# Kernel optimization log

Hardware: AMD Instinct MI355X
Metric: run time of the kernel (lower is better)

## Reference

```python
import jax, jax.numpy as jnp
import numpy as np

N, C, D = 8192, 16, 5

def setup_inputs() -> dict:
    key = jax.random.key(0)
    k1, k2 = jax.random.split(key)
    U = jax.random.normal(k1, (N, C), dtype=jnp.float32)
    ref = jax.random.normal(k2, (N, D), dtype=jnp.float32)
    return {"U": U, "ref": ref}

def reference(U, ref):
    # Exact Gaussian bilateral filter that the permutohedral lattice approximates:
    # out_i = sum_j exp(-0.5 * ||ref_i - ref_j||^2) * U_j  -  U_i
    sq = jnp.sum(ref * ref, axis=-1)                      # [N]
    # squared pairwise distances via gram trick: ||ri||^2 + ||rj||^2 - 2 ri.rj
    d2 = sq[:, None] + sq[None, :] - 2.0 * (ref @ ref.T)  # [N, N]
    W = jnp.exp(-0.5 * jnp.maximum(d2, 0.0))              # [N, N] Gaussian kernel
    return W @ U - U                                      # [N, C]
```

## Files before the change

kernel.cpp:

```cpp
#include <hip/hip_runtime.h>


#define N_ROWS 8192
#define C_CH   16
#define D_DIM  5
#define TPB    256
#define MI     4
#define IPB    (TPB * MI)
#define NIB    (N_ROWS / IPB)
#define NSEG   64
#define JPB    (N_ROWS / NSEG)

#if __has_builtin(__builtin_amdgcn_exp2f)
#define EXP2(x) __builtin_amdgcn_exp2f(x)
#else
#define EXP2(x) exp2f(x)
#endif

#define LOG2E 1.4426950408889634f

__global__ __launch_bounds__(TPB) void lg_main(const float* __restrict__ U,
                                               const float* __restrict__ ref,
                                               float* __restrict__ part) {
    __shared__ float sj[JPB][8];
    __shared__ float su[JPB][16];

    const int bid = blockIdx.x;
    const int ib  = bid % NIB;
    const int seg = bid / NIB;
    const int tid = threadIdx.x;
    const int j0  = seg * JPB;

    const int ibase = ib * IPB + tid;
    float r[MI][D_DIM];
#pragma unroll
    for (int q = 0; q < MI; ++q) {
        const int i = ibase + q * TPB;
#pragma unroll
        for (int d = 0; d < D_DIM; ++d) r[q][d] = ref[i * D_DIM + d];
    }

    if (tid < JPB) {
        const int j = j0 + tid;
        const float v0 = ref[j * D_DIM + 0];
        const float v1 = ref[j * D_DIM + 1];
        const float v2 = ref[j * D_DIM + 2];
        const float v3 = ref[j * D_DIM + 3];
        const float v4 = ref[j * D_DIM + 4];
        float s = v0 * v0;
        s = fmaf(v1, v1, s); s = fmaf(v2, v2, s);
        s = fmaf(v3, v3, s); s = fmaf(v4, v4, s);
        sj[tid][0] = v0 * LOG2E; sj[tid][1] = v1 * LOG2E;
        sj[tid][2] = v2 * LOG2E; sj[tid][3] = v3 * LOG2E;
        sj[tid][4] = v4 * LOG2E; sj[tid][5] = -0.5f * LOG2E * s;
        sj[tid][6] = 0.0f;       sj[tid][7] = 0.0f;
    }
    {
        const float4* __restrict__ U4 = reinterpret_cast<const float4*>(U);
        float4* su4 = reinterpret_cast<float4*>(&su[0][0]);
#pragma unroll
        for (int k = 0; k < (JPB * 4) / TPB; ++k) {
            const int idx = k * TPB + tid;
            su4[idx] = U4[(size_t)j0 * 4 + idx];
        }
    }
    __syncthreads();

    float a[MI];
#pragma unroll
    for (int q = 0; q < MI; ++q) {
        float s = r[q][0] * r[q][0];
        s = fmaf(r[q][1], r[q][1], s); s = fmaf(r[q][2], r[q][2], s);
        s = fmaf(r[q][3], r[q][3], s); s = fmaf(r[q][4], r[q][4], s);
        a[q] = -0.5f * LOG2E * s;
    }

    float acc[MI][C_CH];
#pragma unroll
    for (int q = 0; q < MI; ++q)
#pragma unroll
        for (int c = 0; c < C_CH; ++c) acc[q][c] = 0.0f;

#pragma unroll 4
    for (int jj = 0; jj < JPB; ++jj) {
        const float4 sA = *reinterpret_cast<const float4*>(&sj[jj][0]);
        const float2 sB = *reinterpret_cast<const float2*>(&sj[jj][4]);

        float w[MI];
#pragma unroll
        for (int q = 0; q < MI; ++q) {
            float e = a[q] + sB.y;
            e = fmaf(r[q][0], sA.x, e);
            e = fmaf(r[q][1], sA.y, e);
            e = fmaf(r[q][2], sA.z, e);
            e = fmaf(r[q][3], sA.w, e);
            e = fmaf(r[q][4], sB.x, e);
            w[q] = EXP2(e);
        }

        const float4 u0 = *reinterpret_cast<const float4*>(&su[jj][0]);
        const float4 u1 = *reinterpret_cast<const float4*>(&su[jj][4]);
        const float4 u2 = *reinterpret_cast<const float4*>(&su[jj][8]);
        const float4 u3 = *reinterpret_cast<const float4*>(&su[jj][12]);

#pragma unroll
        for (int q = 0; q < MI; ++q) {
            acc[q][0]  = fmaf(w[q], u0.x, acc[q][0]);
            acc[q][1]  = fmaf(w[q], u0.y, acc[q][1]);
            acc[q][2]  = fmaf(w[q], u0.z, acc[q][2]);
            acc[q][3]  = fmaf(w[q], u0.w, acc[q][3]);
            acc[q][4]  = fmaf(w[q], u1.x, acc[q][4]);
            acc[q][5]  = fmaf(w[q], u1.y, acc[q][5]);
            acc[q][6]  = fmaf(w[q], u1.z, acc[q][6]);
            acc[q][7]  = fmaf(w[q], u1.w, acc[q][7]);
            acc[q][8]  = fmaf(w[q], u2.x, acc[q][8]);
            acc[q][9]  = fmaf(w[q], u2.y, acc[q][9]);
            acc[q][10] = fmaf(w[q], u2.z, acc[q][10]);
            acc[q][11] = fmaf(w[q], u2.w, acc[q][11]);
            acc[q][12] = fmaf(w[q], u3.x, acc[q][12]);
            acc[q][13] = fmaf(w[q], u3.y, acc[q][13]);
            acc[q][14] = fmaf(w[q], u3.z, acc[q][14]);
            acc[q][15] = fmaf(w[q], u3.w, acc[q][15]);
        }
    }

    float4* part4 = reinterpret_cast<float4*>(part);
#pragma unroll
    for (int q = 0; q < MI; ++q) {
        const int i = ibase + q * TPB;
#pragma unroll
        for (int cq = 0; cq < 4; ++cq) {
            part4[((size_t)seg * 4 + cq) * N_ROWS + i] =
                make_float4(acc[q][cq * 4 + 0], acc[q][cq * 4 + 1],
                            acc[q][cq * 4 + 2], acc[q][cq * 4 + 3]);
        }
    }
}

__global__ __launch_bounds__(TPB) void lg_reduce(const float* __restrict__ U,
                                                 const float* __restrict__ part,
                                                 float* __restrict__ out) {
    const int t  = blockIdx.x * TPB + threadIdx.x;
    const int i  = t & (N_ROWS - 1);
    const int cq = t >> 13;
    const float4 u = reinterpret_cast<const float4*>(U)[i * 4 + cq];
    float4 s = make_float4(-u.x, -u.y, -u.z, -u.w);
    const float4* p = reinterpret_cast<const float4*>(part);
#pragma unroll 8
    for (int seg = 0; seg < NSEG; ++seg) {
        const float4 v = p[((size_t)seg * 4 + cq) * N_ROWS + i];
        s.x += v.x; s.y += v.y; s.z += v.z; s.w += v.w;
    }
    reinterpret_cast<float4*>(out)[i * 4 + cq] = s;
}


__global__ __launch_bounds__(TPB) void lg_init(const float* __restrict__ U,
                                               float* __restrict__ out) {
    const int idx = blockIdx.x * TPB + threadIdx.x;
    if (idx < N_ROWS * C_CH) out[idx] = -U[idx];
}

__global__ __launch_bounds__(TPB) void lg_main_atomic(const float* __restrict__ U,
                                                      const float* __restrict__ ref,
                                                      float* __restrict__ out) {
    constexpr int NS  = 32;
    constexpr int JP  = N_ROWS / NS;
    constexpr int NI  = N_ROWS / TPB;
    const int bid = blockIdx.x;
    const int ib  = bid % NI;
    const int sg  = bid / NI;
    const int i   = ib * TPB + threadIdx.x;

    const float r0 = ref[i * D_DIM + 0];
    const float r1 = ref[i * D_DIM + 1];
    const float r2 = ref[i * D_DIM + 2];
    const float r3 = ref[i * D_DIM + 3];
    const float r4 = ref[i * D_DIM + 4];

    float acc[C_CH];
#pragma unroll
    for (int c = 0; c < C_CH; ++c) acc[c] = 0.0f;

    const float4* __restrict__ U4 = reinterpret_cast<const float4*>(U);
    const int j0 = sg * JP;
#pragma unroll 4
    for (int j = j0; j < j0 + JP; ++j) {
        const float d0 = r0 - ref[j * D_DIM + 0];
        const float d1 = r1 - ref[j * D_DIM + 1];
        const float d2 = r2 - ref[j * D_DIM + 2];
        const float d3 = r3 - ref[j * D_DIM + 3];
        const float d4 = r4 - ref[j * D_DIM + 4];
        float dsq = d0 * d0;
        dsq = fmaf(d1, d1, dsq); dsq = fmaf(d2, d2, dsq);
        dsq = fmaf(d3, d3, dsq); dsq = fmaf(d4, d4, dsq);
        const float w = __expf(-0.5f * dsq);

        const float4 u0 = U4[j * 4 + 0];
        const float4 u1 = U4[j * 4 + 1];
        const float4 u2 = U4[j * 4 + 2];
        const float4 u3 = U4[j * 4 + 3];
        acc[0]  = fmaf(w, u0.x, acc[0]);   acc[1]  = fmaf(w, u0.y, acc[1]);
        acc[2]  = fmaf(w, u0.z, acc[2]);   acc[3]  = fmaf(w, u0.w, acc[3]);
        acc[4]  = fmaf(w, u1.x, acc[4]);   acc[5]  = fmaf(w, u1.y, acc[5]);
        acc[6]  = fmaf(w, u1.z, acc[6]);   acc[7]  = fmaf(w, u1.w, acc[7]);
        acc[8]  = fmaf(w, u2.x, acc[8]);   acc[9]  = fmaf(w, u2.y, acc[9]);
        acc[10] = fmaf(w, u2.z, acc[10]);  acc[11] = fmaf(w, u2.w, acc[11]);
        acc[12] = fmaf(w, u3.x, acc[12]);  acc[13] = fmaf(w, u3.y, acc[13]);
        acc[14] = fmaf(w, u3.z, acc[14]);  acc[15] = fmaf(w, u3.w, acc[15]);
    }

    float* o = out + (size_t)i * C_CH;
#pragma unroll
    for (int c = 0; c < C_CH; ++c) atomicAdd(&o[c], acc[c]);
}

extern "C" void kernel_launch(void* const* d_in, const int* in_sizes, int n_in,
                              void* d_out, int out_size, void* d_ws, size_t ws_size,
                              hipStream_t stream) {
    const float* U   = (const float*)d_in[0];
    const float* ref = (const float*)d_in[1];
    float* out       = (float*)d_out;

    const size_t need = (size_t)NSEG * N_ROWS * C_CH * sizeof(float);

    if (ws_size >= need) {
        float* part = (float*)d_ws;
        hipLaunchKernelGGL(lg_main, dim3(NIB * NSEG), dim3(TPB), 0, stream,
                           U, ref, part);
        hipLaunchKernelGGL(lg_reduce, dim3(N_ROWS * C_CH / 4 / TPB), dim3(TPB),
                           0, stream, U, part, out);
    } else {
        hipLaunchKernelGGL(lg_init, dim3((N_ROWS * C_CH + TPB - 1) / TPB), dim3(TPB),
                           0, stream, U, out);
        hipLaunchKernelGGL(lg_main_atomic, dim3((N_ROWS / TPB) * 32), dim3(TPB),
                           0, stream, U, ref, out);
    }
}
```

Measured before the change: 107.8 us.

## Halve rows per thread and software-pipeline LDS loads in main loop

Reduces rows per thread from four to two, which doubles the number of blocks and frees registers for more occupancy. The inner loop is rewritten to double-buffer the shared-memory loads of the next j entry while computing the current one, and the shared arrays gain one padding row so the final prefetch stays in bounds. The intent is to hide LDS latency and raise occupancy. In exchange each loaded sj/su value is reused across fewer rows, so LDS traffic per FMA doubles.

```diff
diff --git a/kernel.cpp b/kernel.cpp
--- a/kernel.cpp
+++ b/kernel.cpp
@@ -5,7 +5,7 @@
 #define C_CH   16
 #define D_DIM  5
 #define TPB    256
-#define MI     4
+#define MI     2
 #define IPB    (TPB * MI)
 #define NIB    (N_ROWS / IPB)
 #define NSEG   64
@@ -22,8 +22,8 @@
 __global__ __launch_bounds__(TPB) void lg_main(const float* __restrict__ U,
                                                const float* __restrict__ ref,
                                                float* __restrict__ part) {
-    __shared__ float sj[JPB][8];
-    __shared__ float su[JPB][16];
+    __shared__ float sj[JPB + 1][8];
+    __shared__ float su[JPB + 1][16];
 
     const int bid = blockIdx.x;
     const int ib  = bid % NIB;
@@ -31,14 +31,13 @@
     const int tid = threadIdx.x;
     const int j0  = seg * JPB;
 
-    const int ibase = ib * IPB + tid;
-    float r[MI][D_DIM];
-#pragma unroll
-    for (int q = 0; q < MI; ++q) {
-        const int i = ibase + q * TPB;
-#pragma unroll
-        for (int d = 0; d < D_DIM; ++d) r[q][d] = ref[i * D_DIM + d];
-    }
+    const int i0 = ib * IPB + tid;
+    const int i1 = i0 + TPB;
+    const float r00 = ref[i0 * D_DIM + 0], r10 = ref[i1 * D_DIM + 0];
+    const float r01 = ref[i0 * D_DIM + 1], r11 = ref[i1 * D_DIM + 1];
+    const float r02 = ref[i0 * D_DIM + 2], r12 = ref[i1 * D_DIM + 2];
+    const float r03 = ref[i0 * D_DIM + 3], r13 = ref[i1 * D_DIM + 3];
+    const float r04 = ref[i0 * D_DIM + 4], r14 = ref[i1 * D_DIM + 4];
 
     if (tid < JPB) {
         const int j = j0 + tid;
@@ -61,79 +60,88 @@
 #pragma unroll
         for (int k = 0; k < (JPB * 4) / TPB; ++k) {
             const int idx = k * TPB + tid;
-            su4[idx] = U4[(size_t)j0 * 4 + idx];
+            su4[(idx / 4) * 4 + (idx & 3)] = U4[(size_t)j0 * 4 + idx];
         }
     }
     __syncthreads();
 
-    float a[MI];
-#pragma unroll
-    for (int q = 0; q < MI; ++q) {
-        float s = r[q][0] * r[q][0];
-        s = fmaf(r[q][1], r[q][1], s); s = fmaf(r[q][2], r[q][2], s);
-        s = fmaf(r[q][3], r[q][3], s); s = fmaf(r[q][4], r[q][4], s);
-        a[q] = -0.5f * LOG2E * s;
-    }
-
-    float acc[MI][C_CH];
-#pragma unroll
-    for (int q = 0; q < MI; ++q)
-#pragma unroll
-        for (int c = 0; c < C_CH; ++c) acc[q][c] = 0.0f;
-
-#pragma unroll 4
-    for (int jj = 0; jj < JPB; ++jj) {
-        const float4 sA = *reinterpret_cast<const float4*>(&sj[jj][0]);
-        const float2 sB = *reinterpret_cast<const float2*>(&sj[jj][4]);
-
-        float w[MI];
-#pragma unroll
-        for (int q = 0; q < MI; ++q) {
-            float e = a[q] + sB.y;
-            e = fmaf(r[q][0], sA.x, e);
-            e = fmaf(r[q][1], sA.y, e);
-            e = fmaf(r[q][2], sA.z, e);
-            e = fmaf(r[q][3], sA.w, e);
-            e = fmaf(r[q][4], sB.x, e);
-            w[q] = EXP2(e);
-        }
-
-        const float4 u0 = *reinterpret_cast<const float4*>(&su[jj][0]);
-        const float4 u1 = *reinterpret_cast<const float4*>(&su[jj][4]);
-        const float4 u2 = *reinterpret_cast<const float4*>(&su[jj][8]);
-        const float4 u3 = *reinterpret_cast<const float4*>(&su[jj][12]);
-
-#pragma unroll
-        for (int q = 0; q < MI; ++q) {
-            acc[q][0]  = fmaf(w[q], u0.x, acc[q][0]);
-            acc[q][1]  = fmaf(w[q], u0.y, acc[q][1]);
-            acc[q][2]  = fmaf(w[q], u0.z, acc[q][2]);
-            acc[q][3]  = fmaf(w[q], u0.w, acc[q][3]);
-            acc[q][4]  = fmaf(w[q], u1.x, acc[q][4]);
-            acc[q][5]  = fmaf(w[q], u1.y, acc[q][5]);
-            acc[q][6]  = fmaf(w[q], u1.z, acc[q][6]);
-            acc[q][7]  = fmaf(w[q], u1.w, acc[q][7]);
-            acc[q][8]  = fmaf(w[q], u2.x, acc[q][8]);
-            acc[q][9]  = fmaf(w[q], u2.y, acc[q][9]);
-            acc[q][10] = fmaf(w[q], u2.z, acc[q][10]);
-            acc[q][11] = fmaf(w[q], u2.w, acc[q][11]);
-            acc[q][12] = fmaf(w[q], u3.x, acc[q][12]);
-            acc[q][13] = fmaf(w[q], u3.y, acc[q][13]);
-            acc[q][14] = fmaf(w[q], u3.z, acc[q][14]);
-            acc[q][15] = fmaf(w[q], u3.w, acc[q][15]);
-        }
-    }
+    float a0 = r00 * r00, a1 = r10 * r10;
+    a0 = fmaf(r01, r01, a0); a1 = fmaf(r11, r11, a1);
+    a0 = fmaf(r02, r02, a0); a1 = fmaf(r12, r12, a1);
+    a0 = fmaf(r03, r03, a0); a1 = fmaf(r13, r13, a1);
+    a0 = fmaf(r04, r04, a0); a1 = fmaf(r14, r14, a1);
+    a0 *= -0.5f * LOG2E;     a1 *= -0.5f * LOG2E;
+
+    float acc0[C_CH], acc1[C_CH];
+#pragma unroll
+    for (int c = 0; c < C_CH; ++c) { acc0[c] = 0.0f; acc1[c] = 0.0f; }
+
+#define LG_COMPUTE(sA, sB, u0, u1, u2, u3)                                   \
+    {                                                                        \
+        float e0 = a0 + sB.y;                                                \
+        float e1 = a1 + sB.y;                                                \
+        e0 = fmaf(r00, sA.x, e0);  e1 = fmaf(r10, sA.x, e1);                 \
+        e0 = fmaf(r01, sA.y, e0);  e1 = fmaf(r11, sA.y, e1);                 \
+        e0 = fmaf(r02, sA.z, e0);  e1 = fmaf(r12, sA.z, e1);                 \
+        e0 = fmaf(r03, sA.w, e0);  e1 = fmaf(r13, sA.w, e1);                 \
+        e0 = fmaf(r04, sB.x, e0);  e1 = fmaf(r14, sB.x, e1);                 \
+        const float w0 = EXP2(e0);                                           \
+        const float w1 = EXP2(e1);                                           \
+        acc0[0]  = fmaf(w0, u0.x, acc0[0]);  acc1[0]  = fmaf(w1, u0.x, acc1[0]); \
+        acc0[1]  = fmaf(w0, u0.y, acc0[1]);  acc1[1]  = fmaf(w1, u0.y, acc1[1]); \
+        acc0[2]  = fmaf(w0, u0.z, acc0[2]);  acc1[2]  = fmaf(w1, u0.z, acc1[2]); \
+        acc0[3]  = fmaf(w0, u0.w, acc0[3]);  acc1[3]  = fmaf(w1, u0.w, acc1[3]); \
+        acc0[4]  = fmaf(w0, u1.x, acc0[4]);  acc1[4]  = fmaf(w1, u1.x, acc1[4]); \
+        acc0[5]  = fmaf(w0, u1.y, acc0[5]);  acc1[5]  = fmaf(w1, u1.y, acc1[5]); \
+        acc0[6]  = fmaf(w0, u1.z, acc0[6]);  acc1[6]  = fmaf(w1, u1.z, acc1[6]); \
+        acc0[7]  = fmaf(w0, u1.w, acc0[7]);  acc1[7]  = fmaf(w1, u1.w, acc1[7]); \
+        acc0[8]  = fmaf(w0, u2.x, acc0[8]);  acc1[8]  = fmaf(w1, u2.x, acc1[8]); \
+        acc0[9]  = fmaf(w0, u2.y, acc0[9]);  acc1[9]  = fmaf(w1, u2.y, acc1[9]); \
+        acc0[10] = fmaf(w0, u2.z, acc0[10]); acc1[10] = fmaf(w1, u2.z, acc1[10]); \
+        acc0[11] = fmaf(w0, u2.w, acc0[11]); acc1[11] = fmaf(w1, u2.w, acc1[11]); \
+        acc0[12] = fmaf(w0, u3.x, acc0[12]); acc1[12] = fmaf(w1, u3.x, acc1[12]); \
+        acc0[13] = fmaf(w0, u3.y, acc0[13]); acc1[13] = fmaf(w1, u3.y, acc1[13]); \
+        acc0[14] = fmaf(w0, u3.z, acc0[14]); acc1[14] = fmaf(w1, u3.z, acc1[14]); \
+        acc0[15] = fmaf(w0, u3.w, acc0[15]); acc1[15] = fmaf(w1, u3.w, acc1[15]); \
+    }
+
+    float4 pA = *reinterpret_cast<const float4*>(&sj[0][0]);
+    float2 pB = *reinterpret_cast<const float2*>(&sj[0][4]);
+    float4 pu0 = *reinterpret_cast<const float4*>(&su[0][0]);
+    float4 pu1 = *reinterpret_cast<const float4*>(&su[0][4]);
+    float4 pu2 = *reinterpret_cast<const float4*>(&su[0][8]);
+    float4 pu3 = *reinterpret_cast<const float4*>(&su[0][12]);
+
+    for (int jj = 0; jj < JPB; jj += 2) {
+        const float4 qA  = *reinterpret_cast<const float4*>(&sj[jj + 1][0]);
+        const float2 qB  = *reinterpret_cast<const float2*>(&sj[jj + 1][4]);
+        const float4 qu0 = *reinterpret_cast<const float4*>(&su[jj + 1][0]);
+        const float4 qu1 = *reinterpret_cast<const float4*>(&su[jj + 1][4]);
+        const float4 qu2 = *reinterpret_cast<const float4*>(&su[jj + 1][8]);
+        const float4 qu3 = *reinterpret_cast<const float4*>(&su[jj + 1][12]);
+
+        LG_COMPUTE(pA, pB, pu0, pu1, pu2, pu3);
+
+        pA  = *reinterpret_cast<const float4*>(&sj[jj + 2][0]);
+        pB  = *reinterpret_cast<const float2*>(&sj[jj + 2][4]);
+        pu0 = *reinterpret_cast<const float4*>(&su[jj + 2][0]);
+        pu1 = *reinterpret_cast<const float4*>(&su[jj + 2][4]);
+        pu2 = *reinterpret_cast<const float4*>(&su[jj + 2][8]);
+        pu3 = *reinterpret_cast<const float4*>(&su[jj + 2][12]);
+
+        LG_COMPUTE(qA, qB, qu0, qu1, qu2, qu3);
+    }
+#undef LG_COMPUTE
 
     float4* part4 = reinterpret_cast<float4*>(part);
 #pragma unroll
-    for (int q = 0; q < MI; ++q) {
-        const int i = ibase + q * TPB;
-#pragma unroll
-        for (int cq = 0; cq < 4; ++cq) {
-            part4[((size_t)seg * 4 + cq) * N_ROWS + i] =
-                make_float4(acc[q][cq * 4 + 0], acc[q][cq * 4 + 1],
-                            acc[q][cq * 4 + 2], acc[q][cq * 4 + 3]);
-        }
+    for (int cq = 0; cq < 4; ++cq) {
+        part4[((size_t)seg * 4 + cq) * N_ROWS + i0] =
+            make_float4(acc0[cq * 4 + 0], acc0[cq * 4 + 1],
+                        acc0[cq * 4 + 2], acc0[cq * 4 + 3]);
+        part4[((size_t)seg * 4 + cq) * N_ROWS + i1] =
+            make_float4(acc1[cq * 4 + 0], acc1[cq * 4 + 1],
+                        acc1[cq * 4 + 2], acc1[cq * 4 + 3]);
     }
 }
 
```

Result: no change. 106.9 us (-0.8%).
